# Kernel tuning notes

Measured on AMD Instinct MI355X. Metric: run time of the kernel, lower is better.

Reference implementation:

```python
import jax, jax.numpy as jnp
import numpy as np

N_NODES = 100000
N_EDGES = 3200000
D_FEAT = 256
UNITS = 256


def setup_inputs() -> dict:
    key = jax.random.key(0)
    k1, k2, k3, k4, k5 = jax.random.split(key, 5)
    X = jax.random.normal(k1, (N_NODES, D_FEAT), dtype=jnp.float32)
    edge_row = jax.random.randint(k2, (N_EDGES,), 0, N_NODES, dtype=jnp.int64 if jax.config.read('jax_enable_x64') else jnp.int32)
    edge_col = jax.random.randint(k3, (N_EDGES,), 0, N_NODES, dtype=edge_row.dtype)
    edge_val = jax.random.uniform(k4, (N_EDGES,), dtype=jnp.float32)
    W = jax.random.normal(k5, (D_FEAT, UNITS), dtype=jnp.float32) * (1.0 / np.sqrt(D_FEAT))
    b = jnp.zeros((UNITS,), dtype=jnp.float32)
    return {"X": X, "edge_row": edge_row, "edge_col": edge_col,
            "edge_val": edge_val, "W": W, "b": b}


def reference(X, edge_row, edge_col, edge_val, W, b):
    # h = X @ W  (dense GEMM)  [N, units]
    h = X @ W
    # out = A @ h (sparse COO SpMM): out[i] = sum_e val[e] * h[col[e]] for row[e]==i
    msgs = edge_val[:, None] * h[edge_col]          # [E, units] gather + scale
    out = jax.ops.segment_sum(msgs, edge_row, num_segments=X.shape[0])
    out = out + b                                    # bias_add
    return jax.nn.relu(out)                          # activation
```

## Files before the change

### kernel.cpp

```cpp
#include <hip/hip_runtime.h>
#include <hip/hip_bf16.h>

#define N_NODES 100000
#define N_EDGES 3200000
#define D_FEAT  256
#define UNITS   256

#define BROWS   128
#define NB      782
#define NCHUNK  256
#define EPB     (N_EDGES / NCHUNK)
#define MAXB    6144

using frag_ab = __attribute__((ext_vector_type(8))) short;
using frag_cd = __attribute__((ext_vector_type(4))) float;

__device__ __forceinline__ unsigned short f2bf(float f) {
    union { float f; unsigned int i; } c; c.f = f;
    unsigned int r = c.i + 0x7FFF + ((c.i >> 16) & 1);
    return (unsigned short)(r >> 16);
}

__global__ __launch_bounds__(256) void convert_wt(const float* __restrict__ W,
                                                  unsigned short* __restrict__ Wt) {
    const int n = blockIdx.x, k = threadIdx.x;
    Wt[n * 256 + k] = f2bf(W[k * 256 + n]);
}

__global__ __launch_bounds__(512) void gemm_q(const float* __restrict__ X,
                                              const unsigned short* __restrict__ Wt,
                                              unsigned char* __restrict__ hq,
                                              float* __restrict__ hscale) {
    __shared__ __align__(16) unsigned char smem[32768];
    __shared__ int rowmax_i[128];
    unsigned short* As = (unsigned short*)smem;
    unsigned short* Bs = (unsigned short*)(smem + 8192);
    unsigned char*  qbuf = smem;

    const int t    = threadIdx.x;
    const int lane = t & 63;
    const int wave = t >> 6;
    const int wm   = (wave >> 2) * 64;
    const int wn   = (wave & 3) * 64;
    const int rowBase = blockIdx.x * 128;
    const int lr = lane & 15, lq = lane >> 4;

    if (t < 128) rowmax_i[t] = 0;

    frag_cd acc[4][4];
    #pragma unroll
    for (int i = 0; i < 4; ++i)
        #pragma unroll
        for (int j = 0; j < 4; ++j)
            acc[i][j] = (frag_cd){0.f, 0.f, 0.f, 0.f};

    for (int k0 = 0; k0 < D_FEAT; k0 += 32) {
        #pragma unroll
        for (int cc = 0; cc < 2; ++cc) {
            const int c = t + cc * 512;
            const int r = c >> 3, fo = (c & 7) * 4;
            const int grow = min(rowBase + r, N_NODES - 1);
            const float4 xv = *(const float4*)(X + (size_t)grow * D_FEAT + k0 + fo);
            ushort4 o;
            o.x = f2bf(xv.x); o.y = f2bf(xv.y); o.z = f2bf(xv.z); o.w = f2bf(xv.w);
            *(ushort4*)(As + r * 32 + fo) = o;
        }
        #pragma unroll
        for (int cc = 0; cc < 2; ++cc) {
            const int c = t + cc * 512;
            *(uint4*)(Bs + c * 8) =
                *(const uint4*)(Wt + (size_t)(c >> 2) * 256 + k0 + (c & 3) * 8);
        }
        __syncthreads();

        frag_ab a[4], b[4];
        #pragma unroll
        for (int i = 0; i < 4; ++i)
            a[i] = *(const frag_ab*)(As + (wm + i * 16 + lr) * 32 + lq * 8);
        #pragma unroll
        for (int j = 0; j < 4; ++j)
            b[j] = *(const frag_ab*)(Bs + (wn + j * 16 + lr) * 32 + lq * 8);

        #pragma unroll
        for (int i = 0; i < 4; ++i)
            #pragma unroll
            for (int j = 0; j < 4; ++j)
                acc[i][j] = __builtin_amdgcn_mfma_f32_16x16x32_bf16(
                    a[i], b[j], acc[i][j], 0, 0, 0);
        __syncthreads();
    }

    float pm[4][4];
    #pragma unroll
    for (int i = 0; i < 4; ++i)
        #pragma unroll
        for (int rr = 0; rr < 4; ++rr) {
            float m = fabsf(acc[i][0][rr]);
            m = fmaxf(m, fabsf(acc[i][1][rr]));
            m = fmaxf(m, fabsf(acc[i][2][rr]));
            m = fmaxf(m, fabsf(acc[i][3][rr]));
            pm[i][rr] = m;
        }
    #pragma unroll
    for (int o = 1; o <= 8; o <<= 1)
        #pragma unroll
        for (int i = 0; i < 4; ++i)
            #pragma unroll
            for (int rr = 0; rr < 4; ++rr)
                pm[i][rr] = fmaxf(pm[i][rr], __shfl_xor(pm[i][rr], o));
    if (lr == 0) {
        #pragma unroll
        for (int i = 0; i < 4; ++i)
            #pragma unroll
            for (int rr = 0; rr < 4; ++rr)
                atomicMax(&rowmax_i[wm + i * 16 + lq * 4 + rr],
                          __float_as_int(pm[i][rr]));
    }
    __syncthreads();

    #pragma unroll
    for (int i = 0; i < 4; ++i)
        #pragma unroll
        for (int rr = 0; rr < 4; ++rr) {
            const int row = wm + i * 16 + lq * 4 + rr;
            const float m = __int_as_float(rowmax_i[row]);
            const float inv = (m > 0.f) ? 127.f / m : 0.f;
            #pragma unroll
            for (int j = 0; j < 4; ++j) {
                const int q = (int)rintf(acc[i][j][rr] * inv);
                qbuf[row * 256 + wn + j * 16 + lr] = (unsigned char)(signed char)q;
            }
        }
    __syncthreads();

    #pragma unroll
    for (int cc = 0; cc < 4; ++cc) {
        const int c = t + cc * 512;
        const int row = c >> 4, fo = (c & 15) * 16;
        const int grow = rowBase + row;
        if (grow < N_NODES)
            *(uint4*)(hq + (size_t)grow * 256 + fo) = *(const uint4*)(qbuf + row * 256 + fo);
    }
    if (t < 128 && rowBase + t < N_NODES)
        hscale[rowBase + t] = __int_as_float(rowmax_i[t]) * (1.f / 127.f);
}

__global__ __launch_bounds__(256) void hist_kernel(const int* __restrict__ erow,
                                                   int* __restrict__ hist_g) {
    __shared__ int h[NB];
    const int t = threadIdx.x;
    const int b = blockIdx.x;
    for (int i = t; i < NB; i += 256) h[i] = 0;
    __syncthreads();
    const int base_e = b * EPB;
    for (int i = t; i < EPB; i += 256)
        atomicAdd(&h[erow[base_e + i] >> 7], 1);
    __syncthreads();
    for (int i = t; i < NB; i += 256)
        hist_g[b * NB + i] = h[i];
}

__global__ __launch_bounds__(256) void scan_buckets(const int* __restrict__ hist_g,
                                                    int* __restrict__ cum,
                                                    int* __restrict__ total) {
    const int k = blockIdx.x, t = threadIdx.x;
    __shared__ int p[256];
    const int v = hist_g[t * NB + k];
    p[t] = v;
    __syncthreads();
    for (int d = 1; d < 256; d <<= 1) {
        const int u = (t >= d) ? p[t - d] : 0;
        __syncthreads();
        p[t] += u;
        __syncthreads();
    }
    cum[t * NB + k] = p[t] - v;
    if (t == 255) total[k] = p[255];
}

__global__ __launch_bounds__(1024) void scan_base(const int* __restrict__ total,
                                                  int* __restrict__ base) {
    const int t = threadIdx.x;
    __shared__ int p[1024];
    const int v = (t < NB) ? total[t] : 0;
    p[t] = v;
    __syncthreads();
    for (int d = 1; d < 1024; d <<= 1) {
        const int u = (t >= d) ? p[t - d] : 0;
        __syncthreads();
        p[t] += u;
        __syncthreads();
    }
    if (t < NB) base[t] = p[t] - v;
    if (t == NB - 1) base[NB] = p[t];
}

__global__ __launch_bounds__(256) void scatter_binned(const int* __restrict__ erow,
                                                      const int* __restrict__ ecol,
                                                      const float* __restrict__ eval,
                                                      const float* __restrict__ hscale,
                                                      const int* __restrict__ cum,
                                                      const int* __restrict__ base,
                                                      uint2* __restrict__ binned) {
    __shared__ int cur[NB];
    const int t = threadIdx.x;
    const int b = blockIdx.x;
    for (int i = t; i < NB; i += 256)
        cur[i] = base[i] + cum[b * NB + i];
    __syncthreads();
    const int base_e = b * EPB;
    for (int i = t; i < EPB; i += 256) {
        const int e = base_e + i;
        const int r = erow[e];
        const int c = ecol[e];
        const float v = eval[e] * hscale[c];
        const int k = r >> 7, rl = r & 127;
        const int pos = atomicAdd(&cur[k], 1);
        binned[pos] = make_uint2(((unsigned)rl << 17) | (unsigned)c,
                                 __float_as_uint(v));
    }
}

__global__ __launch_bounds__(256) void sort_local(const uint2* __restrict__ binned,
                                                  const int* __restrict__ base,
                                                  const int* __restrict__ total,
                                                  uint2* __restrict__ sorted,
                                                  int* __restrict__ offs) {
    __shared__ uint2 buf[MAXB];
    __shared__ int lh[BROWS], loff[BROWS], lcur[BROWS];
    const int k = blockIdx.x, t = threadIdx.x;
    const int s = base[k];
    const int cnt = min(total[k], MAXB);

    if (t < BROWS) lh[t] = 0;
    __syncthreads();
    for (int i = t; i < cnt; i += 256)
        atomicAdd(&lh[binned[s + i].x >> 17], 1);
    __syncthreads();
    if (t < BROWS) loff[t] = lh[t];
    __syncthreads();
    for (int d = 1; d < BROWS; d <<= 1) {
        const int u = (t >= d && t < BROWS) ? loff[t - d] : 0;
        __syncthreads();
        if (t < BROWS) loff[t] += u;
        __syncthreads();
    }
    if (t < BROWS) lcur[t] = loff[t] - lh[t];
    __syncthreads();
    for (int i = t; i < cnt; i += 256) {
        const uint2 eo = binned[s + i];
        const int rl = eo.x >> 17;
        const int p = atomicAdd(&lcur[rl], 1);
        buf[p] = make_uint2(eo.x & 0x1FFFF, eo.y);
    }
    __syncthreads();
    for (int i = t; i < cnt; i += 256)
        sorted[s + i] = buf[i];
    const int rowBase = k * BROWS;
    if (t < BROWS && rowBase + t < N_NODES)
        offs[rowBase + t] = s + (loff[t] - lh[t]);
    if (t == 0 && k == NB - 1)
        offs[N_NODES] = N_EDGES;
}

__global__ __launch_bounds__(64) void spmm_rows(const int* __restrict__ offs,
                                                const uint2* __restrict__ sorted,
                                                const unsigned char* __restrict__ hq,
                                                const float* __restrict__ bias,
                                                float* __restrict__ out) {
    const int r = blockIdx.x;
    const int lane = threadIdx.x;
    __shared__ uint2 le[64];
    int s = offs[r];
    const int e = offs[r + 1];
    float a0 = 0.f, a1 = 0.f, a2 = 0.f, a3 = 0.f;

    while (s < e) {
        const int cnt = min(64, e - s);
        if (lane < cnt) {
            uint2 v = sorted[s + lane];
            v.x &= 0x1FFFF;
            le[lane] = v;
        }
        __syncthreads();
        #pragma unroll 4
        for (int j = 0; j < cnt; ++j) {
            const uint2 cv = le[j];
            const float v = __uint_as_float(cv.y);
            const unsigned int w = *(const unsigned int*)(hq + (size_t)cv.x * 256 + lane * 4);
            a0 += v * (float)((int)(signed char)( w        & 0xFF));
            a1 += v * (float)((int)(signed char)((w >> 8)  & 0xFF));
            a2 += v * (float)((int)(signed char)((w >> 16) & 0xFF));
            a3 += v * (float)((int)(signed char)( w >> 24        ));
        }
        __syncthreads();
        s += cnt;
    }

    const float4 b4 = *(const float4*)(bias + lane * 4);
    float4 o;
    o.x = fmaxf(a0 + b4.x, 0.f);
    o.y = fmaxf(a1 + b4.y, 0.f);
    o.z = fmaxf(a2 + b4.z, 0.f);
    o.w = fmaxf(a3 + b4.w, 0.f);
    *(float4*)(out + (size_t)r * 256 + lane * 4) = o;
}

extern "C" void kernel_launch(void* const* d_in, const int* in_sizes, int n_in,
                              void* d_out, int out_size, void* d_ws, size_t ws_size,
                              hipStream_t stream) {
    const float* X    = (const float*)d_in[0];
    const int*   erow = (const int*)  d_in[1];
    const int*   ecol = (const int*)  d_in[2];
    const float* evalv= (const float*)d_in[3];
    const float* W    = (const float*)d_in[4];
    const float* bias = (const float*)d_in[5];
    float* out = (float*)d_out;

    char* ws = (char*)d_ws;
    size_t off = 0;
    auto alloc = [&](size_t bytes) {
        void* p = ws + off;
        off += (bytes + 255) & ~(size_t)255;
        return p;
    };
    unsigned short* Wt     = (unsigned short*)alloc((size_t)D_FEAT * UNITS * 2);
    unsigned char*  hq     = (unsigned char*) alloc((size_t)N_NODES * UNITS);
    float*          hscale = (float*)         alloc((size_t)N_NODES * 4);
    uint2*          binned = (uint2*)         alloc((size_t)N_EDGES * 8);
    uint2*          sorted = (uint2*)         alloc((size_t)N_EDGES * 8);
    int*            hist_g = (int*)           alloc((size_t)NCHUNK * NB * 4);
    int*            cum    = (int*)           alloc((size_t)NCHUNK * NB * 4);
    int*            total  = (int*)           alloc((size_t)NB * 4);
    int*            basep  = (int*)           alloc((size_t)(NB + 1) * 4);
    int*            offs   = (int*)           alloc((size_t)(N_NODES + 1) * 4);

    convert_wt<<<UNITS, 256, 0, stream>>>(W, Wt);
    gemm_q<<<NB, 512, 0, stream>>>(X, Wt, hq, hscale);
    hist_kernel<<<NCHUNK, 256, 0, stream>>>(erow, hist_g);
    scan_buckets<<<NB, 256, 0, stream>>>(hist_g, cum, total);
    scan_base<<<1, 1024, 0, stream>>>(total, basep);
    scatter_binned<<<NCHUNK, 256, 0, stream>>>(erow, ecol, evalv, hscale, cum, basep, binned);
    sort_local<<<NB, 256, 0, stream>>>(binned, basep, total, sorted, offs);
    spmm_rows<<<N_NODES, 64, 0, stream>>>(offs, sorted, hq, bias, out);
}
```

Baseline: 450.5 us.

## Replace two-level bucket sort with direct per-row global atomic CSR build

Replaces the two-level binned counting sort (per-chunk bucket histograms, bucket scans, binned scatter, then a per-bucket local sort in LDS) with a flat CSR build. It counts edges per row with global atomics, runs a three-stage prefix scan over the row counts, and scatters each edge straight into its final slot with a global atomic cursor per row. This drops one full pass over the edge array and the intermediate binned buffer. In exchange it relies on many contended global atomics on random addresses instead of LDS atomics, and the order of edges within a row becomes nondeterministic.

```diff
diff --git a/kernel.cpp b/kernel.cpp
--- a/kernel.cpp
+++ b/kernel.cpp
@@ -6,11 +6,9 @@
 #define D_FEAT  256
 #define UNITS   256
 
-#define BROWS   128
-#define NB      782
-#define NCHUNK  256
-#define EPB     (N_EDGES / NCHUNK)
-#define MAXB    6144
+#define SCAN_CHUNK   1024
+#define SCAN_BLOCKS  ((N_NODES + SCAN_CHUNK - 1) / SCAN_CHUNK)
+#define ATOM_BLOCKS  1024
 
 using frag_ab = __attribute__((ext_vector_type(8))) short;
 using frag_cd = __attribute__((ext_vector_type(4))) float;
@@ -145,44 +143,25 @@
         hscale[rowBase + t] = __int_as_float(rowmax_i[t]) * (1.f / 127.f);
 }
 
-__global__ __launch_bounds__(256) void hist_kernel(const int* __restrict__ erow,
-                                                   int* __restrict__ hist_g) {
-    __shared__ int h[NB];
-    const int t = threadIdx.x;
-    const int b = blockIdx.x;
-    for (int i = t; i < NB; i += 256) h[i] = 0;
-    __syncthreads();
-    const int base_e = b * EPB;
-    for (int i = t; i < EPB; i += 256)
-        atomicAdd(&h[erow[base_e + i] >> 7], 1);
-    __syncthreads();
-    for (int i = t; i < NB; i += 256)
-        hist_g[b * NB + i] = h[i];
-}
-
-__global__ __launch_bounds__(256) void scan_buckets(const int* __restrict__ hist_g,
-                                                    int* __restrict__ cum,
-                                                    int* __restrict__ total) {
-    const int k = blockIdx.x, t = threadIdx.x;
-    __shared__ int p[256];
-    const int v = hist_g[t * NB + k];
-    p[t] = v;
-    __syncthreads();
-    for (int d = 1; d < 256; d <<= 1) {
-        const int u = (t >= d) ? p[t - d] : 0;
-        __syncthreads();
-        p[t] += u;
-        __syncthreads();
-    }
-    cum[t * NB + k] = p[t] - v;
-    if (t == 255) total[k] = p[255];
-}
-
-__global__ __launch_bounds__(1024) void scan_base(const int* __restrict__ total,
-                                                  int* __restrict__ base) {
-    const int t = threadIdx.x;
+__global__ __launch_bounds__(1024) void zero_cnt(int* __restrict__ cnt) {
+    const int i = blockIdx.x * 1024 + threadIdx.x;
+    if (i < N_NODES) cnt[i] = 0;
+}
+
+__global__ __launch_bounds__(256) void hist_rows(const int* __restrict__ erow,
+                                                 int* __restrict__ cnt) {
+    const int stride = ATOM_BLOCKS * 256;
+    for (int e = blockIdx.x * 256 + threadIdx.x; e < N_EDGES; e += stride)
+        atomicAdd(&cnt[erow[e]], 1);
+}
+
+__global__ __launch_bounds__(1024) void scan_chunk(const int* __restrict__ cnt,
+                                                   int* __restrict__ exc,
+                                                   int* __restrict__ btot) {
+    const int b = blockIdx.x, t = threadIdx.x;
+    const int i = b * 1024 + t;
     __shared__ int p[1024];
-    const int v = (t < NB) ? total[t] : 0;
+    const int v = (i < N_NODES) ? cnt[i] : 0;
     p[t] = v;
     __syncthreads();
     for (int d = 1; d < 1024; d <<= 1) {
@@ -191,76 +170,55 @@
         p[t] += u;
         __syncthreads();
     }
-    if (t < NB) base[t] = p[t] - v;
-    if (t == NB - 1) base[NB] = p[t];
-}
-
-__global__ __launch_bounds__(256) void scatter_binned(const int* __restrict__ erow,
+    if (i < N_NODES) exc[i] = p[t] - v;
+    if (t == 1023) btot[b] = p[1023];
+}
+
+__global__ __launch_bounds__(128) void scan_tot(const int* __restrict__ btot,
+                                                int* __restrict__ bbase) {
+    const int t = threadIdx.x;
+    __shared__ int p[128];
+    const int v = (t < SCAN_BLOCKS) ? btot[t] : 0;
+    p[t] = v;
+    __syncthreads();
+    for (int d = 1; d < 128; d <<= 1) {
+        const int u = (t >= d) ? p[t - d] : 0;
+        __syncthreads();
+        p[t] += u;
+        __syncthreads();
+    }
+    if (t < SCAN_BLOCKS) bbase[t] = p[t] - v;
+}
+
+__global__ __launch_bounds__(1024) void scan_final(const int* __restrict__ exc,
+                                                   const int* __restrict__ bbase,
+                                                   const int* __restrict__ cnt,
+                                                   int* __restrict__ offs,
+                                                   int* __restrict__ cur) {
+    const int b = blockIdx.x, t = threadIdx.x;
+    const int i = b * 1024 + t;
+    if (i < N_NODES) {
+        const int o = exc[i] + bbase[b];
+        offs[i] = o;
+        cur[i]  = o;
+        if (i == N_NODES - 1) offs[N_NODES] = o + cnt[i];
+    }
+}
+
+__global__ __launch_bounds__(256) void scatter_direct(const int* __restrict__ erow,
                                                       const int* __restrict__ ecol,
                                                       const float* __restrict__ eval,
                                                       const float* __restrict__ hscale,
-                                                      const int* __restrict__ cum,
-                                                      const int* __restrict__ base,
-                                                      uint2* __restrict__ binned) {
-    __shared__ int cur[NB];
-    const int t = threadIdx.x;
-    const int b = blockIdx.x;
-    for (int i = t; i < NB; i += 256)
-        cur[i] = base[i] + cum[b * NB + i];
-    __syncthreads();
-    const int base_e = b * EPB;
-    for (int i = t; i < EPB; i += 256) {
-        const int e = base_e + i;
+                                                      int* __restrict__ cur,
+                                                      uint2* __restrict__ sorted) {
+    const int stride = ATOM_BLOCKS * 256;
+    for (int e = blockIdx.x * 256 + threadIdx.x; e < N_EDGES; e += stride) {
         const int r = erow[e];
         const int c = ecol[e];
         const float v = eval[e] * hscale[c];
-        const int k = r >> 7, rl = r & 127;
-        const int pos = atomicAdd(&cur[k], 1);
-        binned[pos] = make_uint2(((unsigned)rl << 17) | (unsigned)c,
-                                 __float_as_uint(v));
-    }
-}
-
-__global__ __launch_bounds__(256) void sort_local(const uint2* __restrict__ binned,
-                                                  const int* __restrict__ base,
-                                                  const int* __restrict__ total,
-                                                  uint2* __restrict__ sorted,
-                                                  int* __restrict__ offs) {
-    __shared__ uint2 buf[MAXB];
-    __shared__ int lh[BROWS], loff[BROWS], lcur[BROWS];
-    const int k = blockIdx.x, t = threadIdx.x;
-    const int s = base[k];
-    const int cnt = min(total[k], MAXB);
-
-    if (t < BROWS) lh[t] = 0;
-    __syncthreads();
-    for (int i = t; i < cnt; i += 256)
-        atomicAdd(&lh[binned[s + i].x >> 17], 1);
-    __syncthreads();
-    if (t < BROWS) loff[t] = lh[t];
-    __syncthreads();
-    for (int d = 1; d < BROWS; d <<= 1) {
-        const int u = (t >= d && t < BROWS) ? loff[t - d] : 0;
-        __syncthreads();
-        if (t < BROWS) loff[t] += u;
-        __syncthreads();
-    }
-    if (t < BROWS) lcur[t] = loff[t] - lh[t];
-    __syncthreads();
-    for (int i = t; i < cnt; i += 256) {
-        const uint2 eo = binned[s + i];
-        const int rl = eo.x >> 17;
-        const int p = atomicAdd(&lcur[rl], 1);
-        buf[p] = make_uint2(eo.x & 0x1FFFF, eo.y);
-    }
-    __syncthreads();
-    for (int i = t; i < cnt; i += 256)
-        sorted[s + i] = buf[i];
-    const int rowBase = k * BROWS;
-    if (t < BROWS && rowBase + t < N_NODES)
-        offs[rowBase + t] = s + (loff[t] - lh[t]);
-    if (t == 0 && k == NB - 1)
-        offs[N_NODES] = N_EDGES;
+        const int pos = atomicAdd(&cur[r], 1);
+        sorted[pos] = make_uint2((unsigned)c, __float_as_uint(v));
+    }
 }
 
 __global__ __launch_bounds__(64) void spmm_rows(const int* __restrict__ offs,
@@ -327,20 +285,21 @@
     unsigned short* Wt     = (unsigned short*)alloc((size_t)D_FEAT * UNITS * 2);
     unsigned char*  hq     = (unsigned char*) alloc((size_t)N_NODES * UNITS);
     float*          hscale = (float*)         alloc((size_t)N_NODES * 4);
-    uint2*          binned = (uint2*)         alloc((size_t)N_EDGES * 8);
     uint2*          sorted = (uint2*)         alloc((size_t)N_EDGES * 8);
-    int*            hist_g = (int*)           alloc((size_t)NCHUNK * NB * 4);
-    int*            cum    = (int*)           alloc((size_t)NCHUNK * NB * 4);
-    int*            total  = (int*)           alloc((size_t)NB * 4);
-    int*            basep  = (int*)           alloc((size_t)(NB + 1) * 4);
+    int*            cnt    = (int*)           alloc((size_t)N_NODES * 4);
+    int*            exc    = (int*)           alloc((size_t)N_NODES * 4);
+    int*            btot   = (int*)           alloc((size_t)SCAN_BLOCKS * 4);
+    int*            bbase  = (int*)           alloc((size_t)SCAN_BLOCKS * 4);
+    int*            cur    = (int*)           alloc((size_t)N_NODES * 4);
     int*            offs   = (int*)           alloc((size_t)(N_NODES + 1) * 4);
 
     convert_wt<<<UNITS, 256, 0, stream>>>(W, Wt);
-    gemm_q<<<NB, 512, 0, stream>>>(X, Wt, hq, hscale);
-    hist_kernel<<<NCHUNK, 256, 0, stream>>>(erow, hist_g);
-    scan_buckets<<<NB, 256, 0, stream>>>(hist_g, cum, total);
-    scan_base<<<1, 1024, 0, stream>>>(total, basep);
-    scatter_binned<<<NCHUNK, 256, 0, stream>>>(erow, ecol, evalv, hscale, cum, basep, binned);
-    sort_local<<<NB, 256, 0, stream>>>(binned, basep, total, sorted, offs);
+    gemm_q<<<(N_NODES + 127) / 128, 512, 0, stream>>>(X, Wt, hq, hscale);
+    zero_cnt<<<SCAN_BLOCKS, 1024, 0, stream>>>(cnt);
+    hist_rows<<<ATOM_BLOCKS, 256, 0, stream>>>(erow, cnt);
+    scan_chunk<<<SCAN_BLOCKS, 1024, 0, stream>>>(cnt, exc, btot);
+    scan_tot<<<1, 128, 0, stream>>>(btot, bbase);
+    scan_final<<<SCAN_BLOCKS, 1024, 0, stream>>>(exc, bbase, cnt, offs, cur);
+    scatter_direct<<<ATOM_BLOCKS, 256, 0, stream>>>(erow, ecol, evalv, hscale, cur, sorted);
     spmm_rows<<<N_NODES, 64, 0, stream>>>(offs, sorted, hq, bias, out);
 }
```

New measurement: 619.1 us. 37.4% more time.
